# Kernel tuning notes

Hardware: AMD Instinct MI355X
Metric: run time of the kernel (lower is better)

## Reference

```python
import jax, jax.numpy as jnp
import numpy as np

B, S, D, E = 8, 128, 768, 100

def setup_inputs() -> dict:
    key = jax.random.key(0)
    ks = jax.random.split(key, 7)
    s = 1.0 / np.sqrt(D)  # roughly Linear init scale
    return {
        "x":     jax.random.normal(ks[0], (B, S, D), dtype=jnp.float32),
        "w_lin": jax.random.normal(ks[1], (E, D, D), dtype=jnp.float32) * s,
        "b_lin": jax.random.normal(ks[2], (E, D), dtype=jnp.float32) * s,
        "w1":    jax.random.normal(ks[3], (E, D, D), dtype=jnp.float32) * s,
        "b1":    jax.random.normal(ks[4], (E, D), dtype=jnp.float32) * s,
        "w2":    jax.random.normal(ks[5], (E, D, D), dtype=jnp.float32) * s,
        "b2":    jax.random.normal(ks[6], (E, D), dtype=jnp.float32) * s,
    }

def reference(x, w_lin, b_lin, w1, b1, w2, b2):
    # Torch Linear: y = x @ W.T + b, weights stacked over experts e.
    # Skip branch: [B,S,O,E]
    lin = jnp.einsum('bsd,eod->bsoe', x, w_lin) + b_lin.T[None, None]
    # MLP branch (dropout is identity in eval mode); exact (erf) GELU as nn.GELU default.
    h = jax.nn.gelu(jnp.einsum('bsd,ehd->bseh', x, w1) + b1[None, None], approximate=False)
    mlp = jnp.einsum('bseh,eoh->bsoe', h, w2) + b2.T[None, None]
    # torch.stack([...], dim=-1) -> [B, S, D_out, E]
    return lin + mlp
```

## Files before the change

kernel.cpp:

```cpp
#include <hip/hip_runtime.h>
#include <hip/hip_bf16.h>
#include <cstdint>

typedef __attribute__((ext_vector_type(8))) short short8;
typedef __attribute__((ext_vector_type(4))) float f32x4;
typedef unsigned short u16;
typedef unsigned int u32;

#define Mdim 1024
#define Ddim 768
#define Edim 100
#define DD (Ddim * Ddim)
#define NW8 7372800

__device__ __forceinline__ u16 f2bf(float f) {
  u32 u = __builtin_bit_cast(u32, f);
  u += 0x7fffu + ((u >> 16) & 1u);
  return (u16)(u >> 16);
}
__device__ __forceinline__ float bf2f(u16 h) {
  return __builtin_bit_cast(float, ((u32)h) << 16);
}
__device__ __forceinline__ u32 pack2(float a, float b) {
  return (u32)f2bf(a) | ((u32)f2bf(b) << 16);
}

__device__ __forceinline__ float gelu_f(float v) {
  float v2 = v * v;
  float wv = v * (2.30220795f + 0.10294322f * v2);
  float ew = __builtin_amdgcn_exp2f(wv);
  return v - v * __builtin_amdgcn_rcpf(ew + 1.0f);
}

#define GLL16(gsrc, ldst)                                                        \
  __builtin_amdgcn_global_load_lds(                                             \
      (const __attribute__((address_space(1))) u32*)(gsrc),                     \
      (__attribute__((address_space(3))) u32*)(ldst), 16, 0, 0)

#define VM8 asm volatile("s_waitcnt vmcnt(8)" ::: "memory")
#define VM0 asm volatile("s_waitcnt vmcnt(0)" ::: "memory")
#define LGKM0 asm volatile("s_waitcnt lgkmcnt(0)" ::: "memory")
#define RAW_BAR                                                                  \
  do {                                                                           \
    __builtin_amdgcn_s_barrier();                                                \
    asm volatile("" ::: "memory");                                               \
  } while (0)

__device__ __forceinline__ void cvt8(const float* __restrict__ s, u16* __restrict__ d) {
  const float4 f0 = *(const float4*)(s);
  const float4 f1 = *(const float4*)(s + 4);
  uint4 v;
  v.x = pack2(f0.x, f0.y); v.y = pack2(f0.z, f0.w);
  v.z = pack2(f1.x, f1.y); v.w = pack2(f1.z, f1.w);
  *(uint4*)(d) = v;
}

__global__ __launch_bounds__(256) void k_prep(const float* __restrict__ x,
                                              u16* __restrict__ xb,
                                              const float* __restrict__ w1,
                                              u16* __restrict__ w1b) {
  const int tid = blockIdx.x * 256 + threadIdx.x;
  if (tid < (Mdim * Ddim) / 8) cvt8(x + (size_t)tid * 8, xb + (size_t)tid * 8);
  for (int i = tid; i < NW8; i += 2048 * 256)
    cvt8(w1 + (size_t)i * 8, w1b + (size_t)i * 8);
}

template <int NT>
__device__ __forceinline__ void gemm8(const u16* __restrict__ A0,
                                      const u16* __restrict__ A1,
                                      const u16* __restrict__ B0,
                                      const u16* __restrict__ B1,
                                      u16* lds, f32x4 (&acc)[8][4], const int t) {
  const int w = t >> 6, l = t & 63;
  const int wr = (w >> 2) << 7;
  const int wc = (w & 3) << 6;
  const int lr = l & 15, c4 = l >> 4, r7 = l & 7;
  const int sl0 = ((c4 ^ r7) << 3);
  const int sl1 = (((4 | c4) ^ r7) << 3);
  const size_t soff = (size_t)((w << 5) + (l >> 3)) * Ddim + (((l & 7) ^ (l >> 3)) << 3);

  auto stage_op = [&](const u16* src, int buf, int isB, int kk) {
    u16* d = lds + (buf << 15) + (isB << 14) + (w << 11);
    const u16* s = src + soff + (kk << 6);
#pragma unroll
    for (int i = 0; i < 4; ++i)
      GLL16(s + (size_t)(i << 3) * Ddim, d + (i << 9));
  };
  auto stage = [&](int tt, int isB) {
    const int buf = tt & 1;
    if (NT == 24 && tt >= 12) stage_op(isB ? B1 : A1, buf, isB, tt - 12);
    else                      stage_op(isB ? B0 : A0, buf, isB, tt);
  };

  short8 af[16], bf[4];
  auto rdA = [&](int buf, int half) {
    const u16* ab = lds + (buf << 15) + (wr + (half << 6) + lr) * 64;
#pragma unroll
    for (int m = 0; m < 4; ++m) {
      af[half * 8 + m * 2]     = *(const short8*)(ab + (m << 10) + sl0);
      af[half * 8 + m * 2 + 1] = *(const short8*)(ab + (m << 10) + sl1);
    }
  };
  auto rdB = [&](int buf, int half) {
    const u16* bb = lds + (buf << 15) + 16384 + (wc + (half << 5) + lr) * 64;
#pragma unroll
    for (int n = 0; n < 2; ++n) {
      bf[n * 2]     = *(const short8*)(bb + (n << 10) + sl0);
      bf[n * 2 + 1] = *(const short8*)(bb + (n << 10) + sl1);
    }
  };
  auto q = [&](int mh, int nh) {
    __builtin_amdgcn_s_setprio(1);
#pragma unroll
    for (int m = 0; m < 4; ++m)
#pragma unroll
      for (int n = 0; n < 2; ++n) {
        f32x4 c = acc[mh * 4 + m][nh * 2 + n];
        c = __builtin_amdgcn_mfma_f32_16x16x32_bf16(af[mh * 8 + m * 2],     bf[n * 2],     c, 0, 0, 0);
        c = __builtin_amdgcn_mfma_f32_16x16x32_bf16(af[mh * 8 + m * 2 + 1], bf[n * 2 + 1], c, 0, 0, 0);
        acc[mh * 4 + m][nh * 2 + n] = c;
      }
    __builtin_amdgcn_s_setprio(0);
  };

  stage(0, 1); stage(0, 0);
  stage(1, 1); stage(1, 0);
  VM8;
  RAW_BAR;

#pragma unroll 2
  for (int T = 0; T < NT - 2; ++T) {
    const int buf = T & 1;
    rdA(buf, 0); rdB(buf, 0);
    RAW_BAR; q(0, 0); RAW_BAR;
    rdA(buf, 1);
    RAW_BAR; q(1, 0); RAW_BAR;
    rdB(buf, 1); stage(T + 2, 0);
    RAW_BAR; q(1, 1); RAW_BAR;
    stage(T + 2, 1);
    VM8;
    RAW_BAR; q(0, 1); RAW_BAR;
  }
  {
    const int buf = (NT - 2) & 1;
    rdA(buf, 0); rdB(buf, 0); RAW_BAR; q(0, 0); RAW_BAR;
    rdA(buf, 1);              RAW_BAR; q(1, 0); RAW_BAR;
    rdB(buf, 1);              RAW_BAR; q(1, 1); RAW_BAR;
    VM0; RAW_BAR; q(0, 1); RAW_BAR;
  }
  {
    const int buf = (NT - 1) & 1;
    rdA(buf, 0); rdB(buf, 0); RAW_BAR; q(0, 0); RAW_BAR;
    rdA(buf, 1);              RAW_BAR; q(1, 0); RAW_BAR;
    rdB(buf, 1);              RAW_BAR; q(1, 1); RAW_BAR;
    q(0, 1);
  }
}

template <bool GELU>
__device__ __forceinline__ void epi_store(f32x4 (&acc)[8][4], const float* bias,
                                          u16* lds, u16* gout, int m_base, int n_base,
                                          const int t) {
  const int w = t >> 6, l = t & 63;
  const int lr = l & 15, c4 = l >> 4;
  u16* reg = lds + (w << 13);

  LGKM0;
  __builtin_amdgcn_sched_barrier(0);
  RAW_BAR;

  float bv[4];
#pragma unroll
  for (int nf = 0; nf < 4; ++nf) bv[nf] = bias[(nf << 4) + lr];

#pragma unroll
  for (int mf = 0; mf < 8; ++mf) {
#pragma unroll
    for (int nf = 0; nf < 4; ++nf) {
      const int slot = (nf << 1) + (lr >> 3);
      const int bis = (lr & 7);
#pragma unroll
      for (int j = 0; j < 4; ++j) {
        float v = acc[mf][nf][j] + bv[nf];
        if (GELU) v = gelu_f(v);
        const int row = (mf << 4) + (c4 << 2) + j;
        reg[row * 64 + ((slot ^ (row & 7)) << 3) + bis] = f2bf(v);
      }
    }
  }
  const int g = l >> 3;
  const int phys = ((l & 7) ^ g) << 3;
#pragma unroll
  for (int r = 0; r < 16; ++r) {
    const int row = (r << 3) + g;
    short8 v = *(const short8*)(reg + row * 64 + phys);
    *(short8*)(gout + (size_t)(m_base + row) * Ddim + n_base + ((l & 7) << 3)) = v;
  }
}

__device__ __forceinline__ void decode8(int bid, int& e, int& m0, int& n0) {
  const int s = (bid & 7) * 150 + (bid >> 3);
  e = s / 12;
  const int r = s % 12;
  m0 = (r & 3) << 8;
  n0 = (r >> 2) << 8;
}

__global__ __launch_bounds__(512, 2) void k_h8(const u16* __restrict__ xb,
                                               const u16* __restrict__ w1b,
                                               const float* __restrict__ b1,
                                               u16* __restrict__ hout,
                                               const float* __restrict__ wl,
                                               const float* __restrict__ w2,
                                               u16* __restrict__ wlb,
                                               u16* __restrict__ w2b) {
  __shared__ __align__(16) u16 lds[65536];
  int e, m0, n0;
  decode8(blockIdx.x, e, m0, n0);
  const int t = threadIdx.x;
  f32x4 acc[8][4] = {};
  gemm8<12>(xb + (size_t)m0 * Ddim, nullptr,
            w1b + (size_t)e * DD + (size_t)n0 * Ddim, nullptr, lds, acc, t);

  const int w = t >> 6;
  const int wr = (w >> 2) << 7, wc = (w & 3) << 6;
  epi_store<true>(acc, b1 + (size_t)e * Ddim + n0 + wc, lds,
                  hout + (size_t)e * Mdim * Ddim, m0 + wr, n0 + wc, t);

  const int tid = blockIdx.x * 512 + t;
  for (int i = tid; i < NW8; i += 1200 * 512)
    cvt8(wl + (size_t)i * 8, wlb + (size_t)i * 8);
  for (int i = tid; i < NW8; i += 1200 * 512)
    cvt8(w2 + (size_t)i * 8, w2b + (size_t)i * 8);
}

__global__ __launch_bounds__(512, 2) void k_out8(const u16* __restrict__ xb,
                                                 const u16* __restrict__ hbuf,
                                                 const u16* __restrict__ wlb,
                                                 const float* __restrict__ b_lin,
                                                 const u16* __restrict__ w2b,
                                                 const float* __restrict__ b2,
                                                 u16* __restrict__ tout) {
  __shared__ __align__(16) u16 lds[65536];
  int e, m0, n0;
  decode8(blockIdx.x, e, m0, n0);
  const int t = threadIdx.x;
  f32x4 acc[8][4] = {};
  gemm8<24>(xb + (size_t)m0 * Ddim,
            hbuf + (size_t)e * Mdim * Ddim + (size_t)m0 * Ddim,
            wlb + (size_t)e * DD + (size_t)n0 * Ddim,
            w2b + (size_t)e * DD + (size_t)n0 * Ddim, lds, acc, t);

  const int w = t >> 6, l = t & 63;
  const int wr = (w >> 2) << 7, wc = (w & 3) << 6;
  const int lr = l & 15;
  const float* bm = b2 + (size_t)e * Ddim + n0 + wc;
#pragma unroll
  for (int nf = 0; nf < 4; ++nf) {
    const float bmv = bm[(nf << 4) + lr];
#pragma unroll
    for (int mf = 0; mf < 8; ++mf)
#pragma unroll
      for (int j = 0; j < 4; ++j) acc[mf][nf][j] += bmv;
  }
  epi_store<false>(acc, b_lin + (size_t)e * Ddim + n0 + wc, lds,
                   tout + (size_t)e * Mdim * Ddim, m0 + wr, n0 + wc, t);
}

__global__ __launch_bounds__(256) void k_tr_bf(const u16* __restrict__ tbuf,
                                               float* __restrict__ out) {
  __shared__ __align__(16) u16 tile[100 * 260];
  const int t = threadIdx.x;
  const size_t MD = (size_t)Mdim * Ddim;
  const size_t md0 = (size_t)blockIdx.x * 256;
#pragma unroll
  for (int p = 0; p < 25; ++p) {
    const int e = p * 4 + (t >> 6);
    const int c = (t & 63) * 4;
    uint2 v = *(const uint2*)(tbuf + (size_t)e * MD + md0 + c);
    *(uint2*)(&tile[e * 260 + c]) = v;
  }
  __syncthreads();
  const size_t obase = md0 * 100;
#pragma unroll 5
  for (int i = 0; i < 100; ++i) {
    const int flat = t + i * 256;
    const int mo = (int)(((u32)flat * 5243u) >> 19);
    const int e = flat - mo * 100;
    out[obase + flat] = bf2f(tile[e * 260 + mo]);
  }
}

__global__ void k_cvt(const float* __restrict__ x, u16* __restrict__ xb) {
  size_t i = ((size_t)blockIdx.x * 256 + threadIdx.x) * 4;
  float4 v = *(const float4*)(x + i);
  uint2 r;
  r.x = pack2(v.x, v.y);
  r.y = pack2(v.z, v.w);
  *(uint2*)(xb + i) = r;
}

__device__ __forceinline__ void gemm_phase_f32(const u16* __restrict__ Ag,
                                               const float* __restrict__ Wg,
                                               u16* As, u16* Bs, f32x4 (&acc)[4][4], int t) {
  const int w = t >> 6, l = t & 63;
  const int lrow = l & 15, lk = (l >> 4) << 3;
  const int wr = ((w >> 1) << 6), wc = ((w & 1) << 6);
  for (int kt = 0; kt < Ddim; kt += 32) {
#pragma unroll
    for (int i = 0; i < 2; ++i) {
      GLL16(Ag + (size_t)((w << 5) + (i << 4) + (l >> 2)) * Ddim + kt + ((l & 3) << 3),
            As + (((w << 5) + (i << 4)) << 5));
    }
    {
      const int r = t >> 1, c = (t & 1) << 4;
      const float* src = Wg + (size_t)r * Ddim + kt + c;
      const float4 f0 = *(const float4*)(src);
      const float4 f1 = *(const float4*)(src + 4);
      const float4 f2 = *(const float4*)(src + 8);
      const float4 f3 = *(const float4*)(src + 12);
      uint4 v0, v1;
      v0.x = pack2(f0.x, f0.y); v0.y = pack2(f0.z, f0.w);
      v0.z = pack2(f1.x, f1.y); v0.w = pack2(f1.z, f1.w);
      v1.x = pack2(f2.x, f2.y); v1.y = pack2(f2.z, f2.w);
      v1.z = pack2(f3.x, f3.y); v1.w = pack2(f3.z, f3.w);
      *(uint4*)(&Bs[r * 32 + c]) = v0;
      *(uint4*)(&Bs[r * 32 + c + 8]) = v1;
    }
    __syncthreads();
    short8 af[4], bfr[4];
#pragma unroll
    for (int f = 0; f < 4; ++f) {
      af[f]  = *(const short8*)(&As[(wr + f * 16 + lrow) * 32 + lk]);
      bfr[f] = *(const short8*)(&Bs[(wc + f * 16 + lrow) * 32 + lk]);
    }
#pragma unroll
    for (int fm = 0; fm < 4; ++fm)
#pragma unroll
      for (int fn = 0; fn < 4; ++fn)
        acc[fm][fn] = __builtin_amdgcn_mfma_f32_16x16x32_bf16(af[fm], bfr[fn], acc[fm][fn], 0, 0, 0);
    __syncthreads();
  }
}

__global__ __launch_bounds__(256) void k_h2(const u16* __restrict__ xb,
                                            const float* __restrict__ w1,
                                            const float* __restrict__ b1,
                                            u16* __restrict__ hout, int e_base) {
  __shared__ __align__(16) u16 As[128 * 32];
  __shared__ __align__(16) u16 Bs[128 * 32];
  const int el = blockIdx.x / 48, r = blockIdx.x % 48;
  const int m0 = (r / 6) * 128, n0 = (r % 6) * 128;
  const int e = e_base + el;
  const int t = threadIdx.x, l = t & 63, wv = t >> 6;
  const int wr = (wv >> 1) * 64, wc = (wv & 1) * 64, lrow = l & 15;
  f32x4 acc[4][4] = {};
  gemm_phase_f32(xb + (size_t)m0 * Ddim, w1 + (size_t)e * DD + (size_t)n0 * Ddim, As, Bs, acc, t);
  const float* bias = b1 + (size_t)e * Ddim + n0;
  u16* hb = hout + (size_t)el * Mdim * Ddim;
#pragma unroll
  for (int fm = 0; fm < 4; ++fm) {
    const int mb = m0 + wr + fm * 16 + ((l >> 4) << 2);
#pragma unroll
    for (int fn = 0; fn < 4; ++fn) {
      const int nc = wc + fn * 16 + lrow;
      const float bv = bias[nc];
#pragma unroll
      for (int j = 0; j < 4; ++j) {
        float v = acc[fm][fn][j] + bv;
        v = 0.5f * v * (1.0f + erff(v * 0.7071067811865475f));
        hb[(size_t)(mb + j) * Ddim + n0 + nc] = f2bf(v);
      }
    }
  }
}

__global__ __launch_bounds__(256) void k_out2(
    const u16* __restrict__ xb, const u16* __restrict__ hbuf,
    const float* __restrict__ wl, const float* __restrict__ b_lin,
    const float* __restrict__ w2, const float* __restrict__ b2,
    float* __restrict__ out, int e_base) {
  __shared__ __align__(16) u16 As[128 * 32];
  __shared__ __align__(16) u16 Bs[128 * 32];
  const int el = blockIdx.x / 48, r = blockIdx.x % 48;
  const int m0 = (r / 6) * 128, n0 = (r % 6) * 128;
  const int e = e_base + el;
  const int t = threadIdx.x, l = t & 63, wv = t >> 6;
  const int wr = (wv >> 1) * 64, wc = (wv & 1) * 64, lrow = l & 15;
  f32x4 acc[4][4] = {};
  gemm_phase_f32(xb + (size_t)m0 * Ddim, wl + (size_t)e * DD + (size_t)n0 * Ddim, As, Bs, acc, t);
  gemm_phase_f32(hbuf + (size_t)el * Mdim * Ddim + (size_t)m0 * Ddim,
                 w2 + (size_t)e * DD + (size_t)n0 * Ddim, As, Bs, acc, t);
  const float* bl = b_lin + (size_t)e * Ddim + n0;
  const float* bm = b2 + (size_t)e * Ddim + n0;
#pragma unroll
  for (int fm = 0; fm < 4; ++fm) {
    const int mb = m0 + wr + fm * 16 + ((l >> 4) << 2);
#pragma unroll
    for (int fn = 0; fn < 4; ++fn) {
      const int nc = wc + fn * 16 + lrow;
      const float bv = bl[nc] + bm[nc];
#pragma unroll
      for (int j = 0; j < 4; ++j)
        out[((size_t)(mb + j) * Ddim + n0 + nc) * Edim + e] = acc[fm][fn][j] + bv;
    }
  }
}

extern "C" void kernel_launch(void* const* d_in, const int* in_sizes, int n_in,
                              void* d_out, int out_size, void* d_ws, size_t ws_size,
                              hipStream_t stream) {
  const float* x     = (const float*)d_in[0];
  const float* w_lin = (const float*)d_in[1];
  const float* b_lin = (const float*)d_in[2];
  const float* w1    = (const float*)d_in[3];
  const float* b1    = (const float*)d_in[4];
  const float* w2    = (const float*)d_in[5];
  const float* b2    = (const float*)d_in[6];
  float* out = (float*)d_out;

  const size_t MD = (size_t)Mdim * Ddim;
  const size_t xb_b = MD * 2;
  const size_t w_b  = (size_t)Edim * DD * 2;
  const size_t h_b  = (size_t)Edim * MD * 2;
  const size_t tb_b = h_b;

  char* base = (char*)d_ws;

  if (ws_size >= xb_b + 3 * w_b + h_b + tb_b) {
    u16* xb   = (u16*)base;
    u16* w1b  = (u16*)(base + xb_b);
    u16* wlb  = (u16*)(base + xb_b + w_b);
    u16* w2b  = (u16*)(base + xb_b + 2 * w_b);
    u16* hbuf = (u16*)(base + xb_b + 3 * w_b);
    u16* tbuf = (u16*)(base + xb_b + 3 * w_b + h_b);
    k_prep<<<dim3(2048), dim3(256), 0, stream>>>(x, xb, w1, w1b);
    k_h8<<<dim3(1200), dim3(512), 0, stream>>>(xb, w1b, b1, hbuf, w_lin, w2, wlb, w2b);
    k_out8<<<dim3(1200), dim3(512), 0, stream>>>(xb, hbuf, wlb, b_lin, w2b, b2, tbuf);
    k_tr_bf<<<dim3((u32)(MD / 256)), dim3(256), 0, stream>>>(tbuf, out);
  } else {
    u16* xb = (u16*)base;
    k_cvt<<<dim3((u32)(MD / 1024)), dim3(256), 0, stream>>>(x, xb);
    size_t avail = ws_size > xb_b ? ws_size - xb_b : 0;
    int EC = (int)(avail / (MD * 2));
    if (EC < 1) EC = 1;
    if (EC > Edim) EC = Edim;
    u16* hbuf = (u16*)(base + xb_b);
    for (int e0 = 0; e0 < Edim; e0 += EC) {
      int ne = (Edim - e0) < EC ? (Edim - e0) : EC;
      k_h2<<<dim3(ne * 48), dim3(256), 0, stream>>>(xb, w1, b1, hbuf, e0);
      k_out2<<<dim3(ne * 48), dim3(256), 0, stream>>>(xb, hbuf, w_lin, b_lin, w2, b2,
                                                      out, e0);
    }
  }
}
```

Baseline: 728.6 us.

## Reorder GEMM inner loop to load both B halves, split weight conversion kernel

The GEMM main loop now reads both B fragment halves up front into separate register arrays and reuses a single A half buffer. This reorders the quadrant MFMA sequence and interleaves the next-tile global-to-LDS staging differently, which cuts A fragment register use and changes how LDS reads overlap with compute. The wl/w2 fp32-to-bf16 conversion moves out of the tail of the h kernel into its own launch between the two GEMMs. That gives the h kernel a leaner epilogue, at the cost of an extra kernel launch and a serialised conversion pass.

```diff
diff --git a/kernel.cpp b/kernel.cpp
--- a/kernel.cpp
+++ b/kernel.cpp
@@ -63,6 +63,17 @@
   if (tid < (Mdim * Ddim) / 8) cvt8(x + (size_t)tid * 8, xb + (size_t)tid * 8);
   for (int i = tid; i < NW8; i += 2048 * 256)
     cvt8(w1 + (size_t)i * 8, w1b + (size_t)i * 8);
+}
+
+__global__ __launch_bounds__(256) void k_prep2(const float* __restrict__ wl,
+                                               u16* __restrict__ wlb,
+                                               const float* __restrict__ w2,
+                                               u16* __restrict__ w2b) {
+  const int tid = blockIdx.x * 256 + threadIdx.x;
+  for (int i = tid; i < NW8; i += 2048 * 256) {
+    cvt8(wl + (size_t)i * 8, wlb + (size_t)i * 8);
+    cvt8(w2 + (size_t)i * 8, w2b + (size_t)i * 8);
+  }
 }
 
 template <int NT>
@@ -92,32 +103,32 @@
     else                      stage_op(isB ? B0 : A0, buf, isB, tt);
   };
 
-  short8 af[16], bf[4];
+  short8 af[8], bf0[4], bf1[4];
   auto rdA = [&](int buf, int half) {
     const u16* ab = lds + (buf << 15) + (wr + (half << 6) + lr) * 64;
 #pragma unroll
     for (int m = 0; m < 4; ++m) {
-      af[half * 8 + m * 2]     = *(const short8*)(ab + (m << 10) + sl0);
-      af[half * 8 + m * 2 + 1] = *(const short8*)(ab + (m << 10) + sl1);
+      af[m * 2]     = *(const short8*)(ab + (m << 10) + sl0);
+      af[m * 2 + 1] = *(const short8*)(ab + (m << 10) + sl1);
     }
   };
-  auto rdB = [&](int buf, int half) {
+  auto rdB = [&](int buf, int half, short8 (&bfh)[4]) {
     const u16* bb = lds + (buf << 15) + 16384 + (wc + (half << 5) + lr) * 64;
 #pragma unroll
     for (int n = 0; n < 2; ++n) {
-      bf[n * 2]     = *(const short8*)(bb + (n << 10) + sl0);
-      bf[n * 2 + 1] = *(const short8*)(bb + (n << 10) + sl1);
+      bfh[n * 2]     = *(const short8*)(bb + (n << 10) + sl0);
+      bfh[n * 2 + 1] = *(const short8*)(bb + (n << 10) + sl1);
     }
   };
-  auto q = [&](int mh, int nh) {
+  auto q = [&](int mh, int nh, short8 (&bfh)[4]) {
     __builtin_amdgcn_s_setprio(1);
 #pragma unroll
     for (int m = 0; m < 4; ++m)
 #pragma unroll
       for (int n = 0; n < 2; ++n) {
         f32x4 c = acc[mh * 4 + m][nh * 2 + n];
-        c = __builtin_amdgcn_mfma_f32_16x16x32_bf16(af[mh * 8 + m * 2],     bf[n * 2],     c, 0, 0, 0);
-        c = __builtin_amdgcn_mfma_f32_16x16x32_bf16(af[mh * 8 + m * 2 + 1], bf[n * 2 + 1], c, 0, 0, 0);
+        c = __builtin_amdgcn_mfma_f32_16x16x32_bf16(af[m * 2],     bfh[n * 2],     c, 0, 0, 0);
+        c = __builtin_amdgcn_mfma_f32_16x16x32_bf16(af[m * 2 + 1], bfh[n * 2 + 1], c, 0, 0, 0);
         acc[mh * 4 + m][nh * 2 + n] = c;
       }
     __builtin_amdgcn_s_setprio(0);
@@ -131,29 +142,34 @@
 #pragma unroll 2
   for (int T = 0; T < NT - 2; ++T) {
     const int buf = T & 1;
-    rdA(buf, 0); rdB(buf, 0);
-    RAW_BAR; q(0, 0); RAW_BAR;
+    rdB(buf, 0, bf0); rdB(buf, 1, bf1); rdA(buf, 0);
+    RAW_BAR; q(0, 0, bf0); RAW_BAR;
+    stage(T + 2, 1);
+    RAW_BAR; q(0, 1, bf1); RAW_BAR;
     rdA(buf, 1);
-    RAW_BAR; q(1, 0); RAW_BAR;
-    rdB(buf, 1); stage(T + 2, 0);
-    RAW_BAR; q(1, 1); RAW_BAR;
-    stage(T + 2, 1);
+    RAW_BAR; q(1, 1, bf1); RAW_BAR;
+    stage(T + 2, 0);
     VM8;
-    RAW_BAR; q(0, 1); RAW_BAR;
+    RAW_BAR; q(1, 0, bf0); RAW_BAR;
   }
   {
     const int buf = (NT - 2) & 1;
-    rdA(buf, 0); rdB(buf, 0); RAW_BAR; q(0, 0); RAW_BAR;
-    rdA(buf, 1);              RAW_BAR; q(1, 0); RAW_BAR;
-    rdB(buf, 1);              RAW_BAR; q(1, 1); RAW_BAR;
-    VM0; RAW_BAR; q(0, 1); RAW_BAR;
+    rdB(buf, 0, bf0); rdB(buf, 1, bf1); rdA(buf, 0);
+    RAW_BAR; q(0, 0, bf0); RAW_BAR;
+    RAW_BAR; q(0, 1, bf1); RAW_BAR;
+    rdA(buf, 1);
+    RAW_BAR; q(1, 1, bf1); RAW_BAR;
+    VM0;
+    RAW_BAR; q(1, 0, bf0); RAW_BAR;
   }
   {
     const int buf = (NT - 1) & 1;
-    rdA(buf, 0); rdB(buf, 0); RAW_BAR; q(0, 0); RAW_BAR;
-    rdA(buf, 1);              RAW_BAR; q(1, 0); RAW_BAR;
-    rdB(buf, 1);              RAW_BAR; q(1, 1); RAW_BAR;
-    q(0, 1);
+    rdB(buf, 0, bf0); rdB(buf, 1, bf1); rdA(buf, 0);
+    RAW_BAR; q(0, 0, bf0); RAW_BAR;
+    RAW_BAR; q(0, 1, bf1); RAW_BAR;
+    rdA(buf, 1);
+    RAW_BAR; q(1, 1, bf1); RAW_BAR;
+    q(1, 0, bf0);
   }
 }
 
@@ -206,14 +222,10 @@
   n0 = (r >> 2) << 8;
 }
 
-__global__ __launch_bounds__(512, 2) void k_h8(const u16* __restrict__ xb,
-                                               const u16* __restrict__ w1b,
-                                               const float* __restrict__ b1,
-                                               u16* __restrict__ hout,
-                                               const float* __restrict__ wl,
-                                               const float* __restrict__ w2,
-                                               u16* __restrict__ wlb,
-                                               u16* __restrict__ w2b) {
+__global__ __launch_bounds__(512, 2) void k_h10(const u16* __restrict__ xb,
+                                                const u16* __restrict__ w1b,
+                                                const float* __restrict__ b1,
+                                                u16* __restrict__ hout) {
   __shared__ __align__(16) u16 lds[65536];
   int e, m0, n0;
   decode8(blockIdx.x, e, m0, n0);
@@ -226,21 +238,15 @@
   const int wr = (w >> 2) << 7, wc = (w & 3) << 6;
   epi_store<true>(acc, b1 + (size_t)e * Ddim + n0 + wc, lds,
                   hout + (size_t)e * Mdim * Ddim, m0 + wr, n0 + wc, t);
-
-  const int tid = blockIdx.x * 512 + t;
-  for (int i = tid; i < NW8; i += 1200 * 512)
-    cvt8(wl + (size_t)i * 8, wlb + (size_t)i * 8);
-  for (int i = tid; i < NW8; i += 1200 * 512)
-    cvt8(w2 + (size_t)i * 8, w2b + (size_t)i * 8);
-}
-
-__global__ __launch_bounds__(512, 2) void k_out8(const u16* __restrict__ xb,
-                                                 const u16* __restrict__ hbuf,
-                                                 const u16* __restrict__ wlb,
-                                                 const float* __restrict__ b_lin,
-                                                 const u16* __restrict__ w2b,
-                                                 const float* __restrict__ b2,
-                                                 u16* __restrict__ tout) {
+}
+
+__global__ __launch_bounds__(512, 2) void k_out10(const u16* __restrict__ xb,
+                                                  const u16* __restrict__ hbuf,
+                                                  const u16* __restrict__ wlb,
+                                                  const float* __restrict__ b_lin,
+                                                  const u16* __restrict__ w2b,
+                                                  const float* __restrict__ b2,
+                                                  u16* __restrict__ tout) {
   __shared__ __align__(16) u16 lds[65536];
   int e, m0, n0;
   decode8(blockIdx.x, e, m0, n0);
@@ -435,8 +441,9 @@
     u16* hbuf = (u16*)(base + xb_b + 3 * w_b);
     u16* tbuf = (u16*)(base + xb_b + 3 * w_b + h_b);
     k_prep<<<dim3(2048), dim3(256), 0, stream>>>(x, xb, w1, w1b);
-    k_h8<<<dim3(1200), dim3(512), 0, stream>>>(xb, w1b, b1, hbuf, w_lin, w2, wlb, w2b);
-    k_out8<<<dim3(1200), dim3(512), 0, stream>>>(xb, hbuf, wlb, b_lin, w2b, b2, tbuf);
+    k_h10<<<dim3(1200), dim3(512), 0, stream>>>(xb, w1b, b1, hbuf);
+    k_prep2<<<dim3(2048), dim3(256), 0, stream>>>(w_lin, wlb, w2, w2b);
+    k_out10<<<dim3(1200), dim3(512), 0, stream>>>(xb, hbuf, wlb, b_lin, w2b, b2, tbuf);
     k_tr_bf<<<dim3((u32)(MD / 256)), dim3(256), 0, stream>>>(tbuf, out);
   } else {
     u16* xb = (u16*)base;
```

Result: no change. 735.6 us (+1.0%).
